# Optimization experiments

Hardware: AMD Instinct MI355X
Metric: run time of the kernel (lower is better)

## Reference

```python
import jax, jax.numpy as jnp
import numpy as np

NODE_DIM, MSG_DIM, PROP_DIM, HIDDEN = 64, 64, 32, 128
V, T, S = 10000, 8, 16


def setup_inputs() -> dict:
    key = jax.random.key(0)
    ks = jax.random.split(key, 8)
    in_dim = NODE_DIM + MSG_DIM + 1 + PROP_DIM  # concat width of the attn MLP
    return {
        "h_t": jax.random.normal(ks[0], (V, NODE_DIM), dtype=jnp.float32),
        "messages": jax.random.normal(ks[1], (V, T, S, MSG_DIM), dtype=jnp.float32),
        "tau_values": jax.random.uniform(ks[2], (T,), dtype=jnp.float32),
        "theta": jax.random.normal(ks[3], (V, PROP_DIM), dtype=jnp.float32),
        "W1": jax.random.normal(ks[4], (in_dim, HIDDEN), dtype=jnp.float32) * 0.02,
        "b1": jnp.zeros((HIDDEN,), dtype=jnp.float32),
        "W2": jax.random.normal(ks[5], (HIDDEN, 1), dtype=jnp.float32) * 0.02,
        "b2": jnp.zeros((1,), dtype=jnp.float32),
    }


def reference(h_t, messages, tau_values, theta, W1, b1, W2, b2):
    # Equivalent to concat([h_exp, messages, tau_exp, theta_exp]) @ W1:
    # split W1 by input block and sum the partial projections, avoiding the
    # materialized (V, T, S, node+msg+1+prop) broadcast-concat tensor.
    Wh = W1[:NODE_DIM]                                  # (node_dim, H)
    Wm = W1[NODE_DIM:NODE_DIM + MSG_DIM]                # (msg_dim, H)
    Wt = W1[NODE_DIM + MSG_DIM]                         # (H,) -- the tau row
    Wp = W1[NODE_DIM + MSG_DIM + 1:]                    # (prop_dim, H)

    hidden = (
        jnp.einsum("vtsd,dh->vtsh", messages, Wm)       # (V, T, S, H)
        + (h_t @ Wh)[:, None, None, :]                  # broadcast over T, S
        + tau_values[None, :, None, None] * Wt[None, None, None, :]
        + (theta @ Wp)[:, None, None, :]
        + b1
    )
    hidden = jax.nn.relu(hidden)
    logits = (hidden @ W2 + b2)[..., 0]                 # (V, T, S)
    return logits
```

## Files before the change

### kernel.cpp

```cpp
#include <hip/hip_runtime.h>
#include <hip/hip_bf16.h>

#define VN 10000
#define HID 128

using bf16x8 = __attribute__((ext_vector_type(8))) __bf16;
using f32x4  = __attribute__((ext_vector_type(4))) float;

typedef const __attribute__((address_space(1))) uint32_t gbl_u32;
typedef __attribute__((address_space(3))) uint32_t lds_u32;

__global__ __launch_bounds__(256) void prep_kernel(
    const float* __restrict__ h_t, const float* __restrict__ theta,
    const float* __restrict__ W1, const float* __restrict__ b1,
    float* __restrict__ base, __bf16* __restrict__ wmt)
{
  const int blk = blockIdx.x;
  const int tid = threadIdx.x;
  if (blk < 625) {
    __shared__ __align__(16) float in[16][96];
    const int v0 = blk * 16;
    {
      const float4* src = (const float4*)(h_t + (size_t)v0 * 64);
      float4 f = src[tid];
      int vl = tid >> 4, c = (tid & 15) * 4;
      *(float4*)&in[vl][c] = f;
    }
    if (tid < 128) {
      const float4* src = (const float4*)(theta + (size_t)v0 * 32);
      float4 f = src[tid];
      int vl = tid >> 3, c = 64 + (tid & 7) * 4;
      *(float4*)&in[vl][c] = f;
    }
    __syncthreads();
    const int h = tid & 127;
    const int half = tid >> 7;
    float acc[8];
    const float bb = b1[h];
    #pragma unroll
    for (int k = 0; k < 8; k++) acc[k] = bb;
    #pragma unroll 4
    for (int dc = 0; dc < 16; dc++) {
      const int d = 4 * dc;
      float w0 = W1[(d + 0) * 128 + h];
      float w1 = W1[(d + 1) * 128 + h];
      float w2 = W1[(d + 2) * 128 + h];
      float w3 = W1[(d + 3) * 128 + h];
      #pragma unroll
      for (int k = 0; k < 8; k++) {
        float4 iv = *(const float4*)&in[2 * k + half][d];
        acc[k] += iv.x * w0 + iv.y * w1 + iv.z * w2 + iv.w * w3;
      }
    }
    #pragma unroll 4
    for (int dc = 0; dc < 8; dc++) {
      const int d = 4 * dc;
      float w0 = W1[(129 + d + 0) * 128 + h];
      float w1 = W1[(129 + d + 1) * 128 + h];
      float w2 = W1[(129 + d + 2) * 128 + h];
      float w3 = W1[(129 + d + 3) * 128 + h];
      #pragma unroll
      for (int k = 0; k < 8; k++) {
        float4 iv = *(const float4*)&in[2 * k + half][64 + d];
        acc[k] += iv.x * w0 + iv.y * w1 + iv.z * w2 + iv.w * w3;
      }
    }
    #pragma unroll
    for (int k = 0; k < 8; k++)
      base[(size_t)(v0 + 2 * k + half) * 128 + h] = acc[k];
  } else {
    int j = (blk - 625) * 256 + tid;
    int n = j >> 6, d = j & 63;
    wmt[j] = (__bf16)W1[(64 + d) * 128 + n];
  }
}

__global__ __launch_bounds__(256, 3) void main_kernel(
    const float* __restrict__ messages, const float* __restrict__ tau,
    const float* __restrict__ W1, const float* __restrict__ W2,
    const float* __restrict__ b2, const float* __restrict__ base,
    const __bf16* __restrict__ wmt, float* __restrict__ out)
{
  __shared__ __align__(16) unsigned char lds[33280 + 18432 + 512];
  __bf16* lB = (__bf16*)(lds + 33280);
  float* lOut = (float*)(lds + 33280 + 18432);

  const int v = blockIdx.x;
  const int tid = threadIdx.x;
  const int w = tid >> 6;
  const int lane = tid & 63;
  const int quad = lane >> 4;
  const int l16 = lane & 15;

  const float* msg = messages + (size_t)v * 8192;

  uint4 breg[4];
  {
    const uint4* bsrc = (const uint4*)wmt;
    #pragma unroll
    for (int j = 0; j < 4; j++) breg[j] = bsrc[j * 256 + tid];
  }

  #pragma unroll
  for (int j = 0; j < 8; j++) {
    const float* g = msg + (32 * w + 4 * j) * 64 + lane * 4;
    __builtin_amdgcn_global_load_lds((gbl_u32*)g,
                                     (lds_u32*)(lds + w * 8320 + j * 1040),
                                     16, 0, 0);
  }

  float bb[8], w2v[8], wtv[8];
  #pragma unroll
  for (int nt = 0; nt < 8; nt++) {
    const int n = nt * 16 + l16;
    bb[nt]  = base[(size_t)v * 128 + n];
    w2v[nt] = W2[n];
    wtv[nt] = W1[128 * 128 + n];
  }
  float tv[2];
  tv[0] = tau[2 * w];
  tv[1] = tau[2 * w + 1];
  const float b2v = b2[0];

  #pragma unroll
  for (int j = 0; j < 4; j++) {
    int idx = j * 256 + tid;
    int r = idx >> 3, c = (idx & 7) * 8;
    *(uint4*)&lB[r * 72 + c] = breg[j];
  }

  __syncthreads();

  f32x4 acc[2][8];
  #pragma unroll
  for (int mt = 0; mt < 2; mt++)
    #pragma unroll
    for (int nt = 0; nt < 8; nt++) acc[mt][nt] = (f32x4){0.f, 0.f, 0.f, 0.f};

  #pragma unroll
  for (int ks = 0; ks < 2; ks++) {
    bf16x8 b[8];
    #pragma unroll
    for (int nt = 0; nt < 8; nt++)
      b[nt] = *(const bf16x8*)&lB[(nt * 16 + l16) * 72 + ks * 32 + quad * 8];
    #pragma unroll
    for (int mt = 0; mt < 2; mt++) {
      const int rr = mt * 16 + l16;
      const float4* ap = (const float4*)(lds + w * 8320 + (rr >> 2) * 1040 +
                                         (rr & 3) * 256 + (ks * 32 + quad * 8) * 4);
      float4 f0 = ap[0], f1 = ap[1];
      bf16x8 a;
      a[0] = (__bf16)f0.x; a[1] = (__bf16)f0.y; a[2] = (__bf16)f0.z; a[3] = (__bf16)f0.w;
      a[4] = (__bf16)f1.x; a[5] = (__bf16)f1.y; a[6] = (__bf16)f1.z; a[7] = (__bf16)f1.w;
      #pragma unroll
      for (int nt = 0; nt < 8; nt++)
        acc[mt][nt] = __builtin_amdgcn_mfma_f32_16x16x32_bf16(a, b[nt], acc[mt][nt], 0, 0, 0);
    }
  }

  #pragma unroll
  for (int mt = 0; mt < 2; mt++) {
    float ps[4] = {0.f, 0.f, 0.f, 0.f};
    #pragma unroll
    for (int nt = 0; nt < 8; nt++) {
      const float add = bb[nt] + tv[mt] * wtv[nt];
      f32x4 a4 = acc[mt][nt];
      #pragma unroll
      for (int r = 0; r < 4; r++) {
        float hdn = fmaxf(a4[r] + add, 0.f);
        ps[r] += hdn * w2v[nt];
      }
    }
    #pragma unroll
    for (int off = 1; off < 16; off <<= 1)
      #pragma unroll
      for (int r = 0; r < 4; r++) ps[r] += __shfl_xor(ps[r], off, 64);
    if (l16 == 0) {
      #pragma unroll
      for (int r = 0; r < 4; r++)
        lOut[32 * w + mt * 16 + quad * 4 + r] = ps[r];
    }
  }
  __syncthreads();
  if (tid < 128) out[(size_t)v * 128 + tid] = lOut[tid] + b2v;
}

extern "C" void kernel_launch(void* const* d_in, const int* in_sizes, int n_in,
                              void* d_out, int out_size, void* d_ws, size_t ws_size,
                              hipStream_t stream) {
  const float* h_t      = (const float*)d_in[0];
  const float* messages = (const float*)d_in[1];
  const float* tau      = (const float*)d_in[2];
  const float* theta    = (const float*)d_in[3];
  const float* W1       = (const float*)d_in[4];
  const float* b1       = (const float*)d_in[5];
  const float* W2       = (const float*)d_in[6];
  const float* b2       = (const float*)d_in[7];
  float* out = (float*)d_out;

  float* base = (float*)d_ws;
  __bf16* wmt = (__bf16*)((char*)d_ws + (size_t)VN * HID * sizeof(float));

  prep_kernel<<<625 + 32, 256, 0, stream>>>(h_t, theta, W1, b1, base, wmt);
  main_kernel<<<VN, 256, 0, stream>>>(messages, tau, W1, W2, b2, base, wmt, out);
}
```

Measured before the change: 452.8 us.

## Load message tiles straight into registers instead of staging through LDS

Message rows are now read from global memory directly into registers in the MFMA A-operand layout, replacing the global_load_lds staging buffer. Shared memory shrinks to just the bf16 weight tile, which should allow more resident blocks per CU and more memory parallelism. The final LDS staging and second barrier are also gone: lanes write float4 results straight to global memory. The trade-off is that message loads are now issued after the weight-tile barrier, so less of that latency can overlap, and per-lane 32-byte reads may coalesce less cleanly.

```diff
diff --git a/kernel.cpp b/kernel.cpp
--- a/kernel.cpp
+++ b/kernel.cpp
@@ -6,9 +6,6 @@
 
 using bf16x8 = __attribute__((ext_vector_type(8))) __bf16;
 using f32x4  = __attribute__((ext_vector_type(4))) float;
-
-typedef const __attribute__((address_space(1))) uint32_t gbl_u32;
-typedef __attribute__((address_space(3))) uint32_t lds_u32;
 
 __global__ __launch_bounds__(256) void prep_kernel(
     const float* __restrict__ h_t, const float* __restrict__ theta,
@@ -81,9 +78,7 @@
     const float* __restrict__ b2, const float* __restrict__ base,
     const __bf16* __restrict__ wmt, float* __restrict__ out)
 {
-  __shared__ __align__(16) unsigned char lds[33280 + 18432 + 512];
-  __bf16* lB = (__bf16*)(lds + 33280);
-  float* lOut = (float*)(lds + 33280 + 18432);
+  __shared__ __align__(16) __bf16 lB[128 * 72];
 
   const int v = blockIdx.x;
   const int tid = threadIdx.x;
@@ -92,21 +87,60 @@
   const int quad = lane >> 4;
   const int l16 = lane & 15;
 
-  const float* msg = messages + (size_t)v * 8192;
-
-  uint4 breg[4];
   {
     const uint4* bsrc = (const uint4*)wmt;
-    #pragma unroll
-    for (int j = 0; j < 4; j++) breg[j] = bsrc[j * 256 + tid];
-  }
-
-  #pragma unroll
-  for (int j = 0; j < 8; j++) {
-    const float* g = msg + (32 * w + 4 * j) * 64 + lane * 4;
-    __builtin_amdgcn_global_load_lds((gbl_u32*)g,
-                                     (lds_u32*)(lds + w * 8320 + j * 1040),
-                                     16, 0, 0);
+    uint4 br[4];
+    #pragma unroll
+    for (int j = 0; j < 4; j++) br[j] = bsrc[j * 256 + tid];
+    #pragma unroll
+    for (int j = 0; j < 4; j++) {
+      int idx = j * 256 + tid;
+      int r = idx >> 3, c = (idx & 7) * 8;
+      *(uint4*)&lB[r * 72 + c] = br[j];
+    }
+  }
+  __syncthreads();
+
+  const float* msg = messages + (size_t)v * 8192;
+  float4 araw[2][2][2];
+  #pragma unroll
+  for (int mt = 0; mt < 2; mt++) {
+    #pragma unroll
+    for (int ks = 0; ks < 2; ks++) {
+      const int m = 32 * w + mt * 16 + l16;
+      const float4* p = (const float4*)(msg + m * 64 + ks * 32 + quad * 8);
+      araw[mt][ks][0] = p[0];
+      araw[mt][ks][1] = p[1];
+    }
+  }
+  bf16x8 a[2][2];
+  #pragma unroll
+  for (int mt = 0; mt < 2; mt++) {
+    #pragma unroll
+    for (int ks = 0; ks < 2; ks++) {
+      const float* af = (const float*)&araw[mt][ks][0];
+      #pragma unroll
+      for (int j = 0; j < 8; j++) a[mt][ks][j] = (__bf16)af[j];
+    }
+  }
+
+  f32x4 acc[2][8];
+  #pragma unroll
+  for (int mt = 0; mt < 2; mt++)
+    #pragma unroll
+    for (int nt = 0; nt < 8; nt++) acc[mt][nt] = (f32x4){0.f, 0.f, 0.f, 0.f};
+
+  #pragma unroll
+  for (int ks = 0; ks < 2; ks++) {
+    bf16x8 b[8];
+    #pragma unroll
+    for (int nt = 0; nt < 8; nt++)
+      b[nt] = *(const bf16x8*)&lB[(nt * 16 + l16) * 72 + ks * 32 + quad * 8];
+    #pragma unroll
+    for (int mt = 0; mt < 2; mt++)
+      #pragma unroll
+      for (int nt = 0; nt < 8; nt++)
+        acc[mt][nt] = __builtin_amdgcn_mfma_f32_16x16x32_bf16(a[mt][ks], b[nt], acc[mt][nt], 0, 0, 0);
   }
 
   float bb[8], w2v[8], wtv[8];
@@ -123,42 +157,6 @@
   const float b2v = b2[0];
 
   #pragma unroll
-  for (int j = 0; j < 4; j++) {
-    int idx = j * 256 + tid;
-    int r = idx >> 3, c = (idx & 7) * 8;
-    *(uint4*)&lB[r * 72 + c] = breg[j];
-  }
-
-  __syncthreads();
-
-  f32x4 acc[2][8];
-  #pragma unroll
-  for (int mt = 0; mt < 2; mt++)
-    #pragma unroll
-    for (int nt = 0; nt < 8; nt++) acc[mt][nt] = (f32x4){0.f, 0.f, 0.f, 0.f};
-
-  #pragma unroll
-  for (int ks = 0; ks < 2; ks++) {
-    bf16x8 b[8];
-    #pragma unroll
-    for (int nt = 0; nt < 8; nt++)
-      b[nt] = *(const bf16x8*)&lB[(nt * 16 + l16) * 72 + ks * 32 + quad * 8];
-    #pragma unroll
-    for (int mt = 0; mt < 2; mt++) {
-      const int rr = mt * 16 + l16;
-      const float4* ap = (const float4*)(lds + w * 8320 + (rr >> 2) * 1040 +
-                                         (rr & 3) * 256 + (ks * 32 + quad * 8) * 4);
-      float4 f0 = ap[0], f1 = ap[1];
-      bf16x8 a;
-      a[0] = (__bf16)f0.x; a[1] = (__bf16)f0.y; a[2] = (__bf16)f0.z; a[3] = (__bf16)f0.w;
-      a[4] = (__bf16)f1.x; a[5] = (__bf16)f1.y; a[6] = (__bf16)f1.z; a[7] = (__bf16)f1.w;
-      #pragma unroll
-      for (int nt = 0; nt < 8; nt++)
-        acc[mt][nt] = __builtin_amdgcn_mfma_f32_16x16x32_bf16(a, b[nt], acc[mt][nt], 0, 0, 0);
-    }
-  }
-
-  #pragma unroll
   for (int mt = 0; mt < 2; mt++) {
     float ps[4] = {0.f, 0.f, 0.f, 0.f};
     #pragma unroll
@@ -176,13 +174,11 @@
       #pragma unroll
       for (int r = 0; r < 4; r++) ps[r] += __shfl_xor(ps[r], off, 64);
     if (l16 == 0) {
-      #pragma unroll
-      for (int r = 0; r < 4; r++)
-        lOut[32 * w + mt * 16 + quad * 4 + r] = ps[r];
-    }
-  }
-  __syncthreads();
-  if (tid < 128) out[(size_t)v * 128 + tid] = lOut[tid] + b2v;
+      float4 o;
+      o.x = ps[0] + b2v; o.y = ps[1] + b2v; o.z = ps[2] + b2v; o.w = ps[3] + b2v;
+      *(float4*)(out + (size_t)v * 128 + 32 * w + mt * 16 + quad * 4) = o;
+    }
+  }
 }
 
 extern "C" void kernel_launch(void* const* d_in, const int* in_sizes, int n_in,
```

After: 463.6 us. +2.4%, slower.
